# Optimization experiments

Measured on AMD Instinct MI355X. Metric: run time of the kernel, lower is better.

Reference implementation:

```python
import jax, jax.numpy as jnp
import numpy as np

N = 50000      # nodes
E = 800000     # edges (avg degree 16)
D = 64         # input_dim
L = 64         # latent_dim


def setup_inputs() -> dict:
    key = jax.random.key(0)
    k1, k2, k3, k4, k5, k6 = jax.random.split(key, 6)
    x = jax.random.normal(k1, (N, D), dtype=jnp.float32)
    weight = jax.random.normal(k2, (D, L), dtype=jnp.float32) / np.sqrt(D)
    bias = jax.random.normal(k3, (L,), dtype=jnp.float32) * 0.01
    # strictly positive degrees to keep division well-behaved
    node_degree = jax.random.uniform(k4, (N, 1), dtype=jnp.float32) + 1.0
    edge_src = jax.random.randint(k5, (E,), 0, N, dtype=jnp.int32)
    edge_dst = jax.random.randint(k6, (E,), 0, N, dtype=jnp.int32)
    return {"x": x, "weight": weight, "bias": bias,
            "node_degree": node_degree,
            "edge_src": edge_src, "edge_dst": edge_dst}


def reference(x, weight, bias, node_degree, edge_src, edge_dst):
    # gnn_spmm(adj, x): sparse aggregate over incoming edges -> [N, D]
    agg = jax.ops.segment_sum(x[edge_src], edge_dst, num_segments=N)
    pooled = agg + x                      # residual self-connection
    node_linear = pooled @ weight + bias  # dense projection [N, L]
    normalized = node_linear / node_degree  # normalize_embedding == 2
    return jax.nn.relu(normalized)
```

## Files before the change

### kernel.cpp

```cpp
#include <hip/hip_runtime.h>
#include <hip/hip_fp16.h>

#define N_NODES 50000
#define DIM 64
#define CB 391
#define CAP 2560
#define EPT 12
#define EB (512 * EPT)
#define BINCAP 64

typedef _Float16 half8 __attribute__((ext_vector_type(8)));
typedef float floatx4 __attribute__((ext_vector_type(4)));

#define WS_CURSOR  0
#define WS_COARSE  2048
#define WS_YH      (WS_COARSE + 4003840)

__global__ void __launch_bounds__(512) prep_kernel(
        const float* __restrict__ x, const float* __restrict__ W,
        const int* __restrict__ edge_src, const int* __restrict__ edge_dst,
        int* __restrict__ cursor, unsigned int* __restrict__ coarse,
        _Float16* __restrict__ yh, int E, int pa) {
    int b = blockIdx.x, t = threadIdx.x;
    if (b < pa) {
        __shared__ int lhist[CB];
        __shared__ int lbase[CB];
        for (int i = t; i < CB; i += 512) lhist[i] = 0;
        __syncthreads();

        int base = b * EB;
        unsigned int pk[EPT];
        int bk[EPT];
        #pragma unroll
        for (int j = 0; j < EPT; ++j) {
            int e = base + j * 512 + t;
            bk[j] = -1;
            if (e < E) {
                int s = edge_src[e];
                int d = edge_dst[e];
                bk[j] = d >> 7;
                pk[j] = ((unsigned int)s << 7) | (unsigned int)(d & 127);
                atomicAdd(&lhist[bk[j]], 1);
            }
        }
        __syncthreads();
        for (int i = t; i < CB; i += 512) {
            lbase[i] = atomicAdd(&cursor[i], lhist[i]);
            lhist[i] = 0;
        }
        __syncthreads();
        #pragma unroll
        for (int j = 0; j < EPT; ++j) {
            if (bk[j] >= 0) {
                int r = atomicAdd(&lhist[bk[j]], 1);
                coarse[(size_t)bk[j] * CAP + lbase[bk[j]] + r] = pk[j];
            }
        }
    } else {
        __shared__ _Float16 wh[64 * 80];
        #pragma unroll
        for (int i = 0; i < 8; ++i) {
            int idx = i * 512 + t;
            int k = idx >> 6, n = idx & 63;
            wh[n * 80 + k] = (_Float16)W[idx];
        }
        __syncthreads();

        int wv = t >> 6, lane = t & 63;
        int m = lane & 15, q = lane >> 4;
        int rbase = (b - pa) * 128 + wv * 16;
        int row = rbase + m;
        int rowc = row < N_NODES ? row : N_NODES - 1;
        const float* xp = x + (size_t)rowc * DIM + q * 8;
        float4 f0 = *reinterpret_cast<const float4*>(xp);
        float4 f1 = *reinterpret_cast<const float4*>(xp + 4);
        float4 f2 = *reinterpret_cast<const float4*>(xp + 32);
        float4 f3 = *reinterpret_cast<const float4*>(xp + 36);
        half8 a0 = {(_Float16)f0.x, (_Float16)f0.y, (_Float16)f0.z, (_Float16)f0.w,
                    (_Float16)f1.x, (_Float16)f1.y, (_Float16)f1.z, (_Float16)f1.w};
        half8 a1 = {(_Float16)f2.x, (_Float16)f2.y, (_Float16)f2.z, (_Float16)f2.w,
                    (_Float16)f3.x, (_Float16)f3.y, (_Float16)f3.z, (_Float16)f3.w};

        floatx4 accp[4];
        #pragma unroll
        for (int tt = 0; tt < 4; ++tt) {
            half8 bb0 = *reinterpret_cast<const half8*>(&wh[(tt * 16 + m) * 80 + q * 8]);
            half8 bb1 = *reinterpret_cast<const half8*>(&wh[(tt * 16 + m) * 80 + 32 + q * 8]);
            floatx4 cf = {0.f, 0.f, 0.f, 0.f};
            cf = __builtin_amdgcn_mfma_f32_16x16x32_f16(a0, bb0, cf, 0, 0, 0);
            cf = __builtin_amdgcn_mfma_f32_16x16x32_f16(a1, bb1, cf, 0, 0, 0);
            accp[tt] = cf;
        }
        #pragma unroll
        for (int r = 0; r < 4; ++r) {
            int orow = rbase + q * 4 + r;
            if (orow < N_NODES) {
                #pragma unroll
                for (int tt = 0; tt < 4; ++tt)
                    yh[(size_t)orow * DIM + tt * 16 + m] = (_Float16)accp[tt][r];
            }
        }
    }
}

__global__ void __launch_bounds__(512, 6) fused_kernel(
        const _Float16* __restrict__ yh,
        const float* __restrict__ bias,
        const float* __restrict__ deg,
        const int* __restrict__ cursor,
        const unsigned int* __restrict__ coarse,
        float* __restrict__ out) {
    __shared__ int sedges[64 * BINCAP];
    __shared__ int cur[64];

    int t = threadIdx.x;
    int b = blockIdx.x;
    int bucket = (b >> 4) * 8 + (b & 7);
    int half = (b >> 3) & 1;
    if (bucket >= CB) return;
    int nb = bucket * 128 + half * 64;
    int cnt = cursor[bucket];
    const unsigned int* cbk = coarse + (size_t)bucket * CAP;

    if (t < 64) cur[t] = 0;
    __syncthreads();

    for (int i = t; i < cnt; i += 512) {
        unsigned int e = cbk[i];
        int loc = (int)(e & 127u);
        if ((loc >> 6) == half) {
            int bin = loc & 63;
            int p = atomicAdd(&cur[bin], 1);
            sedges[bin * BINCAP + p] = (int)(e >> 7);
        }
    }
    __syncthreads();

    int g = t >> 3;
    int c = t & 7;
    int node = nb + g;

    float bj[8];
    *reinterpret_cast<float4*>(&bj[0]) = reinterpret_cast<const float4*>(bias)[c * 2];
    *reinterpret_cast<float4*>(&bj[4]) = reinterpret_cast<const float4*>(bias)[c * 2 + 1];

    float acc[8];
    #pragma unroll
    for (int j = 0; j < 8; ++j) acc[j] = 0.f;
    const int* bp = &sedges[g * BINCAP];
    int ct = cur[g];
    int k = 0;
    for (; k + 8 <= ct; k += 8) {
        int sid[8];
        #pragma unroll
        for (int u = 0; u < 8; ++u) sid[u] = bp[k + u];
        half8 v[8];
        #pragma unroll
        for (int u = 0; u < 8; ++u)
            v[u] = *reinterpret_cast<const half8*>(yh + (size_t)sid[u] * DIM + c * 8);
        #pragma unroll
        for (int u = 0; u < 8; ++u) {
            #pragma unroll
            for (int j = 0; j < 8; ++j) acc[j] += (float)v[u][j];
        }
    }
    for (; k + 4 <= ct; k += 4) {
        int sid[4];
        #pragma unroll
        for (int u = 0; u < 4; ++u) sid[u] = bp[k + u];
        half8 v[4];
        #pragma unroll
        for (int u = 0; u < 4; ++u)
            v[u] = *reinterpret_cast<const half8*>(yh + (size_t)sid[u] * DIM + c * 8);
        #pragma unroll
        for (int u = 0; u < 4; ++u) {
            #pragma unroll
            for (int j = 0; j < 8; ++j) acc[j] += (float)v[u][j];
        }
    }
    for (; k < ct; ++k) {
        int s0 = bp[k];
        half8 v0 = *reinterpret_cast<const half8*>(yh + (size_t)s0 * DIM + c * 8);
        #pragma unroll
        for (int j = 0; j < 8; ++j) acc[j] += (float)v0[j];
    }

    if (node < N_NODES) {
        half8 r = *reinterpret_cast<const half8*>(yh + (size_t)node * DIM + c * 8);
        float inv = 1.0f / deg[node];
        float o[8];
        #pragma unroll
        for (int j = 0; j < 8; ++j)
            o[j] = fmaxf((acc[j] + (float)r[j] + bj[j]) * inv, 0.f);
        float4* op = reinterpret_cast<float4*>(out + (size_t)node * DIM + c * 8);
        op[0] = make_float4(o[0], o[1], o[2], o[3]);
        op[1] = make_float4(o[4], o[5], o[6], o[7]);
    }
}

extern "C" void kernel_launch(void* const* d_in, const int* in_sizes, int n_in,
                              void* d_out, int out_size, void* d_ws, size_t ws_size,
                              hipStream_t stream) {
    const float* x        = (const float*)d_in[0];
    const float* weight   = (const float*)d_in[1];
    const float* bias     = (const float*)d_in[2];
    const float* node_deg = (const float*)d_in[3];
    const int*   edge_src = (const int*)d_in[4];
    const int*   edge_dst = (const int*)d_in[5];
    float* out = (float*)d_out;
    const int E = in_sizes[4];

    char* ws = (char*)d_ws;
    int*          cursor = (int*)(ws + WS_CURSOR);
    unsigned int* coarse = (unsigned int*)(ws + WS_COARSE);
    _Float16*     yh     = (_Float16*)(ws + WS_YH);

    hipMemsetAsync(cursor, 0, CB * sizeof(int), stream);

    int pa = (E + EB - 1) / EB;
    prep_kernel<<<pa + 391, 512, 0, stream>>>(
        x, weight, edge_src, edge_dst, cursor, coarse, yh, E, pa);

    fused_kernel<<<784, 512, 0, stream>>>(
        yh, bias, node_deg, cursor, coarse, out);
}
```

Before: 109.5 us.

## Use 64-node buckets and half-precision pairwise summation in gather

Bucket edges at 64-destination granularity so each fused block reads only its own bucket, rather than scanning a 128-node bucket and discarding half of it. The gather loop now sums groups of 8 or 4 neighbor rows in fp16 packed adds before converting to fp32, which cuts conversion and add instructions. The trade-offs are lower accumulation precision, more atomic cursors, and more contention in the prep histogram. The memset still clears only CB ints, which is now 782, and the coarse offset was moved to 4096 to fit them.

```diff
diff --git a/kernel.cpp b/kernel.cpp
--- a/kernel.cpp
+++ b/kernel.cpp
@@ -3,8 +3,8 @@
 
 #define N_NODES 50000
 #define DIM 64
-#define CB 391
-#define CAP 2560
+#define CB 782
+#define CAP 1280
 #define EPT 12
 #define EB (512 * EPT)
 #define BINCAP 64
@@ -13,7 +13,7 @@
 typedef float floatx4 __attribute__((ext_vector_type(4)));
 
 #define WS_CURSOR  0
-#define WS_COARSE  2048
+#define WS_COARSE  4096
 #define WS_YH      (WS_COARSE + 4003840)
 
 __global__ void __launch_bounds__(512) prep_kernel(
@@ -38,8 +38,8 @@
             if (e < E) {
                 int s = edge_src[e];
                 int d = edge_dst[e];
-                bk[j] = d >> 7;
-                pk[j] = ((unsigned int)s << 7) | (unsigned int)(d & 127);
+                bk[j] = d >> 6;
+                pk[j] = ((unsigned int)s << 6) | (unsigned int)(d & 63);
                 atomicAdd(&lhist[bk[j]], 1);
             }
         }
@@ -115,24 +115,18 @@
 
     int t = threadIdx.x;
     int b = blockIdx.x;
-    int bucket = (b >> 4) * 8 + (b & 7);
-    int half = (b >> 3) & 1;
-    if (bucket >= CB) return;
-    int nb = bucket * 128 + half * 64;
-    int cnt = cursor[bucket];
-    const unsigned int* cbk = coarse + (size_t)bucket * CAP;
+    int nb = b * 64;
+    int cnt = cursor[b];
+    const unsigned int* cbk = coarse + (size_t)b * CAP;
 
     if (t < 64) cur[t] = 0;
     __syncthreads();
 
     for (int i = t; i < cnt; i += 512) {
         unsigned int e = cbk[i];
-        int loc = (int)(e & 127u);
-        if ((loc >> 6) == half) {
-            int bin = loc & 63;
-            int p = atomicAdd(&cur[bin], 1);
-            sedges[bin * BINCAP + p] = (int)(e >> 7);
-        }
+        int bin = (int)(e & 63u);
+        int p = atomicAdd(&cur[bin], 1);
+        sedges[bin * BINCAP + p] = (int)(e >> 6);
     }
     __syncthreads();
 
@@ -158,13 +152,17 @@
         #pragma unroll
         for (int u = 0; u < 8; ++u)
             v[u] = *reinterpret_cast<const half8*>(yh + (size_t)sid[u] * DIM + c * 8);
-        #pragma unroll
-        for (int u = 0; u < 8; ++u) {
-            #pragma unroll
-            for (int j = 0; j < 8; ++j) acc[j] += (float)v[u][j];
-        }
-    }
-    for (; k + 4 <= ct; k += 4) {
+        half8 s0 = v[0] + v[1];
+        half8 s1 = v[2] + v[3];
+        half8 s2 = v[4] + v[5];
+        half8 s3 = v[6] + v[7];
+        half8 u0 = s0 + s1;
+        half8 u1 = s2 + s3;
+        half8 w  = u0 + u1;
+        #pragma unroll
+        for (int j = 0; j < 8; ++j) acc[j] += (float)w[j];
+    }
+    if (k + 4 <= ct) {
         int sid[4];
         #pragma unroll
         for (int u = 0; u < 4; ++u) sid[u] = bp[k + u];
@@ -172,11 +170,12 @@
         #pragma unroll
         for (int u = 0; u < 4; ++u)
             v[u] = *reinterpret_cast<const half8*>(yh + (size_t)sid[u] * DIM + c * 8);
-        #pragma unroll
-        for (int u = 0; u < 4; ++u) {
-            #pragma unroll
-            for (int j = 0; j < 8; ++j) acc[j] += (float)v[u][j];
-        }
+        half8 s0 = v[0] + v[1];
+        half8 s1 = v[2] + v[3];
+        half8 u0 = s0 + s1;
+        #pragma unroll
+        for (int j = 0; j < 8; ++j) acc[j] += (float)u0[j];
+        k += 4;
     }
     for (; k < ct; ++k) {
         int s0 = bp[k];
@@ -221,6 +220,6 @@
     prep_kernel<<<pa + 391, 512, 0, stream>>>(
         x, weight, edge_src, edge_dst, cursor, coarse, yh, E, pa);
 
-    fused_kernel<<<784, 512, 0, stream>>>(
+    fused_kernel<<<CB, 512, 0, stream>>>(
         yh, bias, node_deg, cursor, coarse, out);
 }
```

New measurement: 105.2 us. -3.9%, faster.
